# Kernel tuning notes

Hardware: AMD Instinct MI355X
Metric: run time of the kernel (lower is better)

## Reference

```python
import jax, jax.numpy as jnp
import numpy as np

N_NODES = 100000
N_EDGES = 1600000
HIDDEN = 64
N_MID = 3  # num_layers=5 -> 1 first + 3 middle + 1 last


def setup_inputs() -> dict:
    key = jax.random.key(0)
    ks = jax.random.split(key, 12)
    x = jax.random.normal(ks[0], (N_NODES, 1), dtype=jnp.float32)
    edge_index = jax.random.randint(ks[1], (2, N_EDGES), 0, N_NODES, dtype=jnp.int32)
    edge_weight = jax.random.uniform(ks[2], (N_EDGES,), dtype=jnp.float32)
    s0 = 1.0  # fan_in=1
    sh = 1.0 / np.sqrt(HIDDEN)
    Wrel0 = jax.random.normal(ks[3], (HIDDEN, 1), dtype=jnp.float32) * s0
    brel0 = jax.random.normal(ks[4], (HIDDEN,), dtype=jnp.float32) * s0
    Wroot0 = jax.random.normal(ks[5], (HIDDEN, 1), dtype=jnp.float32) * s0
    Wrel_mid = jax.random.normal(ks[6], (N_MID, HIDDEN, HIDDEN), dtype=jnp.float32) * sh
    brel_mid = jax.random.normal(ks[7], (N_MID, HIDDEN), dtype=jnp.float32) * sh
    Wroot_mid = jax.random.normal(ks[8], (N_MID, HIDDEN, HIDDEN), dtype=jnp.float32) * sh
    WrelL = jax.random.normal(ks[9], (1, HIDDEN), dtype=jnp.float32) * sh
    brelL = jax.random.normal(ks[10], (1,), dtype=jnp.float32) * sh
    WrootL = jax.random.normal(ks[11], (1, HIDDEN), dtype=jnp.float32) * sh
    return {"x": x, "edge_index": edge_index, "edge_weight": edge_weight,
            "Wrel0": Wrel0, "brel0": brel0, "Wroot0": Wroot0,
            "Wrel_mid": Wrel_mid, "brel_mid": brel_mid, "Wroot_mid": Wroot_mid,
            "WrelL": WrelL, "brelL": brelL, "WrootL": WrootL}


def reference(x, edge_index, edge_weight, Wrel0, brel0, Wroot0,
              Wrel_mid, brel_mid, Wroot_mid, WrelL, brelL, WrootL):
    src = edge_index[0]
    dst = edge_index[1]
    n = x.shape[0]

    def conv(h, Wrel, brel, Wroot):
        # PyG GraphConv(aggr='add'): lin_rel(sum_j w_ij * h_j) + lin_root(h_i)
        msg = h[src] * edge_weight[:, None]          # [E, C]
        agg = jax.ops.segment_sum(msg, dst, num_segments=n)  # [N, C]
        return agg @ Wrel.T + brel + h @ Wroot.T

    # dropout omitted (deterministic reference); relu after all but last layer
    h = jax.nn.relu(conv(x, Wrel0, brel0, Wroot0))
    for i in range(Wrel_mid.shape[0]):
        h = jax.nn.relu(conv(h, Wrel_mid[i], brel_mid[i], Wroot_mid[i]))
    return conv(h, WrelL, brelL, WrootL)  # [N, 1]
```

## Files before the change

### kernel.cpp

```cpp
#include <hip/hip_runtime.h>
#include <stdint.h>


#define NN 100000
#define NE 1600000
#define HID 64
#define NBKT 391
#define CAP 8192
#define TILE 4096
#define EPT 16
#define NTILE ((NE + TILE - 1) / TILE)

typedef __attribute__((ext_vector_type(8))) short bf16x8;
typedef __attribute__((ext_vector_type(4))) float f32x4;
typedef __attribute__((ext_vector_type(2))) unsigned int u32x2;
typedef __attribute__((ext_vector_type(4))) unsigned int u32x4;

__device__ __forceinline__ uint32_t rne_bf16(float v) {
    uint32_t u = __float_as_uint(v);
    return (u + 0x7fffu + ((u >> 16) & 1u)) >> 16;
}


__global__ __launch_bounds__(256) void k_bpart(const int* __restrict__ src,
                                               const int* __restrict__ dst,
                                               const float* __restrict__ w,
                                               int* __restrict__ bcur,
                                               int2* __restrict__ bpairs) {
    __shared__ int  hcnt[NBKT];
    __shared__ int  hoff[NBKT];
    __shared__ int  hadj[NBKT];
    __shared__ int  sc0[512];
    __shared__ int  sc1[512];
    __shared__ int2 sT[TILE];
    __shared__ int  sAdj[TILE];
    int tile0 = blockIdx.x * TILE;
    int t = threadIdx.x;
    for (int i = t; i < NBKT; i += 256) hcnt[i] = 0;
    __syncthreads();

    int   pk[EPT];
    int   bk[EPT];
    float wv[EPT];
    #pragma unroll
    for (int k = 0; k < EPT; k++) {
        int e = tile0 + t + k * 256;
        if (e < NE) {
            int d = dst[e];
            int b = d >> 8;
            pk[k] = (src[e] << 8) | (d & 255);
            wv[k] = w[e];
            bk[k] = b;
            atomicAdd(&hcnt[b], 1);
        } else {
            bk[k] = -1;
        }
    }
    __syncthreads();

    sc0[t]       = (t < NBKT) ? hcnt[t] : 0;
    sc0[t + 256] = (t + 256 < NBKT) ? hcnt[t + 256] : 0;
    __syncthreads();
    int* cur = sc0;
    int* oth = sc1;
    for (int off = 1; off < 512; off <<= 1) {
        int v0 = cur[t]       + ((t       >= off) ? cur[t - off]       : 0);
        int v1 = cur[t + 256] + ((t + 256 >= off) ? cur[t + 256 - off] : 0);
        oth[t] = v0;
        oth[t + 256] = v1;
        __syncthreads();
        int* tmp = cur; cur = oth; oth = tmp;
    }
    for (int i = t; i < NBKT; i += 256) {
        int c = hcnt[i];
        int excl = cur[i] - c;
        hoff[i] = excl;
        int gbase = c ? atomicAdd(&bcur[i], c) : 0;
        hadj[i] = gbase - excl;
        hcnt[i] = 0;
    }
    __syncthreads();

    #pragma unroll
    for (int k = 0; k < EPT; k++) {
        if (bk[k] >= 0) {
            int b = bk[k];
            int pos = hoff[b] + atomicAdd(&hcnt[b], 1);
            sT[pos] = make_int2(pk[k], __float_as_int(wv[k]));
            sAdj[pos] = hadj[b];
        }
    }
    __syncthreads();

    int n = NE - tile0; if (n > TILE) n = TILE;
    for (int j = t; j < n; j += 256)
        bpairs[sAdj[j] + j] = sT[j];
}

__global__ __launch_bounds__(256) void k_bcsr(const int* __restrict__ bcur,
                                              const int2* __restrict__ bpairs,
                                              int* __restrict__ offs,
                                              int* __restrict__ ends,
                                              uint32_t* __restrict__ pairs) {
    __shared__ int2 sE[CAP];
    __shared__ int cnt[256];
    __shared__ int scn[256];
    __shared__ int cur[256];
    int k = blockIdx.x, t = threadIdx.x;
    int base = k * CAP;
    int scnt = bcur[k] - base;
    cnt[t] = 0;
    __syncthreads();
    for (int j = t; j < scnt; j += 256) {
        int2 q = bpairs[base + j];
        sE[j] = q;
        atomicAdd(&cnt[q.x & 255], 1);
    }
    __syncthreads();
    int v = cnt[t], acc = v;
    scn[t] = v;
    __syncthreads();
    for (int off = 1; off < 256; off <<= 1) {
        int u = (t >= off) ? scn[t - off] : 0;
        __syncthreads();
        acc += u;
        scn[t] = acc;
        __syncthreads();
    }
    int excl = acc - v;
    cur[t] = excl;
    int d = (k << 8) + t;
    if (d < NN) {
        offs[d] = base + excl;
        ends[d] = base + excl + v;
    }
    __syncthreads();
    for (int j = t; j < scnt; j += 256) {
        int2 q = sE[j];
        int pos = base + atomicAdd(&cur[q.x & 255], 1);
        uint32_t wb = rne_bf16(__int_as_float(q.y)) & 0x7fffu;
        pairs[pos] = (wb << 17) | (uint32_t)(q.x >> 8);
    }
}


__global__ __launch_bounds__(256) void k_wsplit(const float* __restrict__ Wrel_mid,
                                                const float* __restrict__ Wroot_mid,
                                                uint16_t* __restrict__ WgH,
                                                uint16_t* __restrict__ WgL,
                                                uint16_t* __restrict__ WrH,
                                                uint16_t* __restrict__ WrL,
                                                int* __restrict__ bcur) {
    int i = blockIdx.x * blockDim.x + threadIdx.x;
    if (i < NBKT) bcur[i] = i * CAP;
    if (i >= 3 * 4096) return;
    float a = Wrel_mid[i];
    uint32_t ah = rne_bf16(a);
    float al = a - __uint_as_float(ah << 16);
    WgH[i] = (uint16_t)ah;
    WgL[i] = (uint16_t)rne_bf16(al);
    float b = Wroot_mid[i];
    uint32_t bh = rne_bf16(b);
    float bl = b - __uint_as_float(bh << 16);
    WrH[i] = (uint16_t)bh;
    WrL[i] = (uint16_t)rne_bf16(bl);
}


__device__ __forceinline__ void mfma_epilogue(
        int lane, int w, const uint32_t* sH,
        const uint16_t* __restrict__ WgH, const uint16_t* __restrict__ WgL,
        const uint16_t* __restrict__ WrH, const uint16_t* __restrict__ WrL,
        const float* __restrict__ brel,
        uint16_t* sG, uint16_t* sR) {
    int row = lane & 15;
    int quad = lane >> 4;
    int kb = quad * 8;
    bf16x8 ah0 = *(const bf16x8*)&sH[row * 36 + quad * 4];
    bf16x8 ah1 = *(const bf16x8*)&sH[row * 36 + 16 + quad * 4];
    int oc = w * 16 + row;
    {
        bf16x8 bh0 = *(const bf16x8*)&WgH[oc * 64 + kb];
        bf16x8 bh1 = *(const bf16x8*)&WgH[oc * 64 + 32 + kb];
        bf16x8 bl0 = *(const bf16x8*)&WgL[oc * 64 + kb];
        bf16x8 bl1 = *(const bf16x8*)&WgL[oc * 64 + 32 + kb];
        f32x4 acc = {0.f, 0.f, 0.f, 0.f};
        acc = __builtin_amdgcn_mfma_f32_16x16x32_bf16(ah0, bh0, acc, 0, 0, 0);
        acc = __builtin_amdgcn_mfma_f32_16x16x32_bf16(ah1, bh1, acc, 0, 0, 0);
        acc = __builtin_amdgcn_mfma_f32_16x16x32_bf16(ah0, bl0, acc, 0, 0, 0);
        acc = __builtin_amdgcn_mfma_f32_16x16x32_bf16(ah1, bl1, acc, 0, 0, 0);
        #pragma unroll
        for (int r = 0; r < 4; r++)
            sG[(quad * 4 + r) * 68 + oc] = (uint16_t)rne_bf16(acc[r]);
    }
    {
        bf16x8 bh0 = *(const bf16x8*)&WrH[oc * 64 + kb];
        bf16x8 bh1 = *(const bf16x8*)&WrH[oc * 64 + 32 + kb];
        bf16x8 bl0 = *(const bf16x8*)&WrL[oc * 64 + kb];
        bf16x8 bl1 = *(const bf16x8*)&WrL[oc * 64 + 32 + kb];
        float bias = brel[oc];
        f32x4 acc = {bias, bias, bias, bias};
        acc = __builtin_amdgcn_mfma_f32_16x16x32_bf16(ah0, bh0, acc, 0, 0, 0);
        acc = __builtin_amdgcn_mfma_f32_16x16x32_bf16(ah1, bh1, acc, 0, 0, 0);
        acc = __builtin_amdgcn_mfma_f32_16x16x32_bf16(ah0, bl0, acc, 0, 0, 0);
        acc = __builtin_amdgcn_mfma_f32_16x16x32_bf16(ah1, bl1, acc, 0, 0, 0);
        #pragma unroll
        for (int r = 0; r < 4; r++)
            sR[(quad * 4 + r) * 68 + oc] = (uint16_t)rne_bf16(acc[r]);
    }
}

__device__ __forceinline__ void epilogue_writeout(
        int tid, int blk16, const uint16_t* sG, const uint16_t* sR,
        uint16_t* __restrict__ Gout, uint16_t* __restrict__ Rout) {
    const uint32_t* sGd = (const uint32_t*)sG;
    const uint32_t* sRd = (const uint32_t*)sR;
    uint32_t* Gd = (uint32_t*)Gout;
    uint32_t* Rd = (uint32_t*)Rout;
    #pragma unroll
    for (int it = 0; it < 2; it++) {
        int idx = it * 256 + tid;
        int nd = idx >> 5, col = idx & 31;
        Gd[(blk16 + nd) * 32 + col] = sGd[nd * 34 + col];
        Rd[(blk16 + nd) * 32 + col] = sRd[nd * 34 + col];
    }
}


__global__ __launch_bounds__(256) void k_l0pre(
        const int* __restrict__ offs, const int* __restrict__ ends,
        const uint32_t* __restrict__ pairs, const float* __restrict__ x,
        const float* __restrict__ Wrel0, const float* __restrict__ brel0,
        const float* __restrict__ Wroot0,
        const uint16_t* __restrict__ WgH, const uint16_t* __restrict__ WgL,
        const uint16_t* __restrict__ WrH, const uint16_t* __restrict__ WrL,
        const float* __restrict__ brel,
        uint16_t* __restrict__ Gout, uint16_t* __restrict__ Rout) {
    __shared__ uint32_t sH[16 * 36];
    __shared__ uint16_t sG[16 * 68];
    __shared__ uint16_t sR[16 * 68];
    int c = threadIdx.x & 63;
    int w = threadIdx.x >> 6;
    int blk16 = blockIdx.x * 16;
    float agg[4];
    #pragma unroll
    for (int t = 0; t < 4; t++) {
        int node = blk16 + w * 4 + t;
        int b = offs[node], e = ends[node];
        float pp = 0.f;
        for (int j = b + c; j < e; j += 64) {
            uint32_t r = pairs[j];
            pp += __uint_as_float((r >> 17) << 16) * x[r & 0x1ffffu];
        }
        for (int o = 32; o > 0; o >>= 1) pp += __shfl_down(pp, o, 64);
        agg[t] = __shfl(pp, 0, 64);
    }
    float wr = Wrel0[c], br = brel0[c], wo = Wroot0[c];
    #pragma unroll
    for (int t = 0; t < 4; t++) {
        int node = blk16 + w * 4 + t;
        float v = agg[t] * wr + br + x[node] * wo;
        v = v > 0.f ? v : 0.f;
        uint32_t hb = rne_bf16(v);
        uint32_t pn = (uint32_t)__shfl_xor((int)hb, 1, 64);
        if (!(c & 1)) sH[(w * 4 + t) * 36 + (c >> 1)] = hb | (pn << 16);
    }
    __syncthreads();
    mfma_epilogue(c, w, sH, WgH, WgL, WrH, WrL, brel, sG, sR);
    __syncthreads();
    epilogue_writeout((int)threadIdx.x, blk16, sG, sR, Gout, Rout);
}

#define TRR(dst, off) \
    asm volatile("ds_read_b64_tr_b16 %0, %1 offset:" #off \
                 : "=v"(dst) : "v"(trb))

template <bool LAST>
__global__ __launch_bounds__(256, 6) void k_aggfused(
        const int* __restrict__ offs, const int* __restrict__ ends,
        const uint32_t* __restrict__ pairs,
        const uint16_t* __restrict__ Gb, const uint16_t* __restrict__ Rb,
        const uint16_t* __restrict__ WgH, const uint16_t* __restrict__ WgL,
        const uint16_t* __restrict__ WrH, const uint16_t* __restrict__ WrL,
        const float* __restrict__ brel,
        uint16_t* __restrict__ Gout, uint16_t* __restrict__ Rout,
        const float* __restrict__ WrelL, const float* __restrict__ WrootL,
        float* __restrict__ sarr, float* __restrict__ rarr) {
    __shared__ uint32_t sH[16 * 36];
    __shared__ __align__(128) char smem[16384];
    int c = threadIdx.x & 63;
    int w = threadIdx.x >> 6;
    int blk16 = blockIdx.x * 16;
    int n0 = blk16 + w * 4;
    int ov = 0;
    if (c < 4) ov = offs[n0 + c];
    else if (c == 4) ov = ends[n0 + 3];
    int bnd[5];
    bnd[0] = __builtin_amdgcn_readlane(ov, 0);
    bnd[1] = __builtin_amdgcn_readlane(ov, 1);
    bnd[2] = __builtin_amdgcn_readlane(ov, 2);
    bnd[3] = __builtin_amdgcn_readlane(ov, 3);
    bnd[4] = __builtin_amdgcn_readlane(ov, 4);

    int arow  = c & 15;
    int kq    = (c >> 4) * 8;
    int eprm  = ((c >> 5) << 2) | ((c >> 1) & 3);
    int lbyte = ((c >> 3) & 3) * 32 + (c & 1) * 16;
    char* stg = smem + w * 4096;
    uint32_t stgOff = (uint32_t)(uintptr_t)
        (__attribute__((address_space(3))) char*)stg;
    uint32_t trb = stgOff + ((uint32_t)(c >> 4) << 10)
                          + ((uint32_t)(c & 15) << 3);

    int blo = bnd[0], bhi = bnd[1];
    if (arow == 1) { blo = bnd[1]; bhi = bnd[2]; }
    if (arow == 2) { blo = bnd[2]; bhi = bnd[3]; }
    if (arow == 3) { blo = bnd[3]; bhi = bnd[4]; }
    if (arow >= 4) { blo = 0;      bhi = 0;      }
    uint32_t wid = (uint32_t)(bhi - blo);

    {
        f32x4 z = {0.f, 0.f, 0.f, 0.f};
        #pragma unroll
        for (int i = 0; i < 4; i++)
            *(f32x4*)(stg + i * 1024 + c * 16) = z;
        asm volatile("s_waitcnt lgkmcnt(0)" ::: "memory");
    }

    f32x4 acc16[4];
    {
        int ur[4];
        #pragma unroll
        for (int t = 0; t < 4; t++) ur[t] = (int)(uint32_t)Rb[(n0 + t) * 64 + c];
        #pragma unroll
        for (int nb = 0; nb < 4; nb++) {
            int idx = (nb * 16 + (c & 15)) * 4;
            f32x4 ci;
            #pragma unroll
            for (int t = 0; t < 4; t++) {
                uint32_t rv = (uint32_t)__builtin_amdgcn_ds_bpermute(idx, ur[t]);
                ci[t] = __uint_as_float(rv << 16);
            }
            acc16[nb] = ci;
        }
    }

    const char* gbase = (const char*)Gb;
    uint32_t p = 0;
    if (bnd[0] + c < bnd[4]) p = pairs[bnd[0] + c];

    for (int cb = bnd[0]; cb < bnd[4]; cb += 64) {
        uint32_t pnext = 0;
        if (cb + 64 + c < bnd[4]) pnext = pairs[cb + 64 + c];
        #pragma unroll
        for (int s = 0; s < 2; s++) {
            int sb = cb + s * 32;
            if (sb < bnd[4]) {
                int sn = bnd[4] - sb; if (sn > 32) sn = 32;
                int ni = (sn + 7) >> 3;
                int es4 = (s * 32 + eprm) * 4;
                #pragma unroll
                for (int i = 0; i < 4; i++) {
                    if (i < ni) {
                        uint32_t r = (uint32_t)__builtin_amdgcn_ds_bpermute(
                            es4 + i * 32, (int)p);
                        uint32_t voff = ((r & 0x1ffffu) << 7) + (uint32_t)lbyte;
                        __builtin_amdgcn_global_load_lds(
                            (const __attribute__((address_space(1))) void*)(gbase + voff),
                            (__attribute__((address_space(3))) void*)(stg + i * 1024),
                            16, 0, 0);
                    }
                }
                asm volatile("s_waitcnt vmcnt(0)" ::: "memory");
                u32x2 tb0, tb1, tb2, tb3, tb4, tb5, tb6, tb7;
                TRR(tb0, 0);   TRR(tb1, 512);
                TRR(tb2, 128); TRR(tb3, 640);
                TRR(tb4, 256); TRR(tb5, 768);
                TRR(tb6, 384); TRR(tb7, 896);
                int kidx = s * 128 + kq * 4;
                int db = sb + kq - blo;
                uint32_t m[8];
                #pragma unroll
                for (int q = 0; q < 8; q++) {
                    uint32_t rq = (uint32_t)__builtin_amdgcn_ds_bpermute(
                        kidx + q * 4, (int)p);
                    uint32_t bf = rq >> 17;
                    m[q] = ((uint32_t)(db + q) < wid) ? bf : 0u;
                }
                u32x4 aa = { m[0] | (m[1] << 16), m[2] | (m[3] << 16),
                             m[4] | (m[5] << 16), m[6] | (m[7] << 16) };
                bf16x8 af = __builtin_bit_cast(bf16x8, aa);
                asm volatile("s_waitcnt lgkmcnt(0)" ::: "memory");
                __builtin_amdgcn_sched_barrier(0);
                {
                    u32x4 bb0 = { tb0.x, tb0.y, tb1.x, tb1.y };
                    acc16[0] = __builtin_amdgcn_mfma_f32_16x16x32_bf16(
                        af, __builtin_bit_cast(bf16x8, bb0), acc16[0], 0, 0, 0);
                    u32x4 bb1 = { tb2.x, tb2.y, tb3.x, tb3.y };
                    acc16[1] = __builtin_amdgcn_mfma_f32_16x16x32_bf16(
                        af, __builtin_bit_cast(bf16x8, bb1), acc16[1], 0, 0, 0);
                    u32x4 bb2 = { tb4.x, tb4.y, tb5.x, tb5.y };
                    acc16[2] = __builtin_amdgcn_mfma_f32_16x16x32_bf16(
                        af, __builtin_bit_cast(bf16x8, bb2), acc16[2], 0, 0, 0);
                    u32x4 bb3 = { tb6.x, tb6.y, tb7.x, tb7.y };
                    acc16[3] = __builtin_amdgcn_mfma_f32_16x16x32_bf16(
                        af, __builtin_bit_cast(bf16x8, bb3), acc16[3], 0, 0, 0);
                }
            }
        }
        p = pnext;
    }

    if (!LAST) {
        #pragma unroll
        for (int t = 0; t < 4; t++) {
            #pragma unroll
            for (int nb = 0; nb < 4; nb++) {
                float v = acc16[nb][t];
                v = v > 0.f ? v : 0.f;
                uint32_t hb = rne_bf16(v);
                uint32_t pn2 = (uint32_t)__shfl_xor((int)hb, 1, 64);
                if (!(c & 1) && c < 16)
                    sH[(w * 4 + t) * 36 + nb * 8 + (c >> 1)] = hb | (pn2 << 16);
            }
        }
        __syncthreads();
        uint16_t* sG = (uint16_t*)smem;
        uint16_t* sR = (uint16_t*)(smem + 2176);
        mfma_epilogue(c, w, sH, WgH, WgL, WrH, WrL, brel, sG, sR);
        __syncthreads();
        epilogue_writeout((int)threadIdx.x, blk16, sG, sR, Gout, Rout);
    } else {
        float wl[4], wo[4];
        #pragma unroll
        for (int nb = 0; nb < 4; nb++) {
            wl[nb] = WrelL[nb * 16 + (c & 15)];
            wo[nb] = WrootL[nb * 16 + (c & 15)];
        }
        #pragma unroll
        for (int t = 0; t < 4; t++) {
            float pa = 0.f, pr = 0.f;
            #pragma unroll
            for (int nb = 0; nb < 4; nb++) {
                float v = acc16[nb][t];
                v = v > 0.f ? v : 0.f;
                pa += v * wl[nb];
                pr += v * wo[nb];
            }
            #pragma unroll
            for (int o = 8; o > 0; o >>= 1) {
                pa += __shfl_down(pa, o, 64);
                pr += __shfl_down(pr, o, 64);
            }
            if (c == 0) { sarr[n0 + t] = pa; rarr[n0 + t] = pr; }
        }
    }
}

__global__ void k_last(const int* __restrict__ offs, const int* __restrict__ ends,
                       const uint32_t* __restrict__ pairs,
                       const float* __restrict__ sarr, const float* __restrict__ rarr,
                       const float* __restrict__ brelL, float* __restrict__ out) {
    int i = blockIdx.x * blockDim.x + threadIdx.x;
    if (i >= NN) return;
    float a0 = rarr[i] + brelL[0], a1 = 0.f;
    int b = offs[i], e = ends[i];
    int j = b;
    for (; j + 2 <= e; j += 2) {
        uint32_t r0 = pairs[j], r1 = pairs[j + 1];
        a0 += __uint_as_float((r0 >> 17) << 16) * sarr[r0 & 0x1ffffu];
        a1 += __uint_as_float((r1 >> 17) << 16) * sarr[r1 & 0x1ffffu];
    }
    for (; j < e; j++) {
        uint32_t r = pairs[j];
        a0 += __uint_as_float((r >> 17) << 16) * sarr[r & 0x1ffffu];
    }
    out[i] = a0 + a1;
}

extern "C" void kernel_launch(void* const* d_in, const int* in_sizes, int n_in,
                              void* d_out, int out_size, void* d_ws, size_t ws_size,
                              hipStream_t stream) {
    const float* x        = (const float*)d_in[0];
    const int*   ei       = (const int*)d_in[1];
    const float* ew       = (const float*)d_in[2];
    const float* Wrel0    = (const float*)d_in[3];
    const float* brel0    = (const float*)d_in[4];
    const float* Wroot0   = (const float*)d_in[5];
    const float* Wrel_mid = (const float*)d_in[6];
    const float* brel_mid = (const float*)d_in[7];
    const float* Wroot_mid= (const float*)d_in[8];
    const float* WrelL    = (const float*)d_in[9];
    const float* brelL    = (const float*)d_in[10];
    const float* WrootL   = (const float*)d_in[11];
    float* out = (float*)d_out;

    const int* src  = ei;
    const int* dstp = ei + NE;

    char* w = (char*)d_ws;
    size_t o = 0;
    auto alloc = [&](size_t b) -> void* {
        void* r = (void*)(w + o);
        o += (b + 255) & ~(size_t)255;
        return r;
    };
    int*      offs  = (int*)alloc((size_t)NN * 4);
    int*      ends  = (int*)alloc((size_t)NN * 4);
    int*      bcur  = (int*)alloc((size_t)NBKT * 4);
    uint16_t* WgH   = (uint16_t*)alloc((size_t)3 * 4096 * 2);
    uint16_t* WgL   = (uint16_t*)alloc((size_t)3 * 4096 * 2);
    uint16_t* WrH   = (uint16_t*)alloc((size_t)3 * 4096 * 2);
    uint16_t* WrL   = (uint16_t*)alloc((size_t)3 * 4096 * 2);
    float*    sarr  = (float*)alloc((size_t)NN * 4);
    float*    rarr  = (float*)alloc((size_t)NN * 4);
    uint32_t* pairs = (uint32_t*)alloc((size_t)NBKT * CAP * 4);
    uint16_t* GbA   = (uint16_t*)alloc((size_t)NN * HID * 2);
    uint16_t* RbA   = (uint16_t*)alloc((size_t)NN * HID * 2);
    uint16_t* GbB   = (uint16_t*)alloc((size_t)NN * HID * 2);
    uint16_t* RbB   = (uint16_t*)alloc((size_t)NN * HID * 2);
    (void)RbB;
    int2*  bpairs = (int2*)GbB;

    k_wsplit<<<(3 * 4096 + 255) / 256, 256, 0, stream>>>(
        Wrel_mid, Wroot_mid, WgH, WgL, WrH, WrL, bcur);

    k_bpart<<<NTILE, 256, 0, stream>>>(src, dstp, ew, bcur, bpairs);
    k_bcsr<<<NBKT, 256, 0, stream>>>(bcur, bpairs, offs, ends, pairs);

    k_l0pre<<<NN / 16, 256, 0, stream>>>(
        offs, ends, pairs, x, Wrel0, brel0, Wroot0,
        WgH, WgL, WrH, WrL, brel_mid, GbA, RbA);

    k_aggfused<false><<<NN / 16, 256, 0, stream>>>(
        offs, ends, pairs, GbA, RbA,
        WgH + 4096, WgL + 4096, WrH + 4096, WrL + 4096, brel_mid + HID,
        GbB, RbB, WrelL, WrootL, sarr, rarr);
    k_aggfused<false><<<NN / 16, 256, 0, stream>>>(
        offs, ends, pairs, GbB, RbB,
        WgH + 2 * 4096, WgL + 2 * 4096, WrH + 2 * 4096, WrL + 2 * 4096,
        brel_mid + 2 * HID, GbA, RbA, WrelL, WrootL, sarr, rarr);
    k_aggfused<true><<<NN / 16, 256, 0, stream>>>(
        offs, ends, pairs, GbA, RbA,
        WgH, WgL, WrH, WrL, brel_mid,
        GbB, RbB, WrelL, WrootL, sarr, rarr);

    k_last<<<(NN + 255) / 256, 256, 0, stream>>>(offs, ends, pairs, sarr, rarr, brelL, out);
}
```

Before: 319.9 us.

## Double-buffer edge gathers in aggregation loop and warp-per-node final layer

The fused aggregation loop now issues both 32-edge halves of each 64-edge chunk into two separate LDS staging buffers before waiting. It then consumes the first half after a partial vmcnt wait while the second half's loads are still in flight. Per-half guards and the staging-buffer zero-fill are gone; out-of-range lanes gather row 0 and are masked through zero weights, and the pairs prefetch index is clamped. Doubling LDS per block lowers the occupancy hint from 6 to 4, and k_last is rewritten so each wavefront reduces one node's edges cooperatively instead of one thread per node.

Measured after the change: 324.4 us. Within noise of the previous version (+1.4%).

```diff
diff --git a/kernel.cpp b/kernel.cpp
--- a/kernel.cpp
+++ b/kernel.cpp
@@ -7,6 +7,7 @@
 #define HID 64
 #define NBKT 391
 #define CAP 8192
+#define PMAX (NBKT * CAP)
 #define TILE 4096
 #define EPT 16
 #define NTILE ((NE + TILE - 1) / TILE)
@@ -271,12 +272,15 @@
     epilogue_writeout((int)threadIdx.x, blk16, sG, sR, Gout, Rout);
 }
 
-#define TRR(dst, off) \
+#define TRRA(dst, off) \
     asm volatile("ds_read_b64_tr_b16 %0, %1 offset:" #off \
-                 : "=v"(dst) : "v"(trb))
+                 : "=v"(dst) : "v"(trbA))
+#define TRRB(dst, off) \
+    asm volatile("ds_read_b64_tr_b16 %0, %1 offset:" #off \
+                 : "=v"(dst) : "v"(trbB))
 
 template <bool LAST>
-__global__ __launch_bounds__(256, 6) void k_aggfused(
+__global__ __launch_bounds__(256, 4) void k_aggfused(
         const int* __restrict__ offs, const int* __restrict__ ends,
         const uint32_t* __restrict__ pairs,
         const uint16_t* __restrict__ Gb, const uint16_t* __restrict__ Rb,
@@ -287,7 +291,7 @@
         const float* __restrict__ WrelL, const float* __restrict__ WrootL,
         float* __restrict__ sarr, float* __restrict__ rarr) {
     __shared__ uint32_t sH[16 * 36];
-    __shared__ __align__(128) char smem[16384];
+    __shared__ __align__(128) char smem[32768];
     int c = threadIdx.x & 63;
     int w = threadIdx.x >> 6;
     int blk16 = blockIdx.x * 16;
@@ -306,11 +310,12 @@
     int kq    = (c >> 4) * 8;
     int eprm  = ((c >> 5) << 2) | ((c >> 1) & 3);
     int lbyte = ((c >> 3) & 3) * 32 + (c & 1) * 16;
-    char* stg = smem + w * 4096;
+    char* stg = smem + w * 8192;
     uint32_t stgOff = (uint32_t)(uintptr_t)
         (__attribute__((address_space(3))) char*)stg;
-    uint32_t trb = stgOff + ((uint32_t)(c >> 4) << 10)
+    uint32_t trbA = stgOff + ((uint32_t)(c >> 4) << 10)
                           + ((uint32_t)(c & 15) << 3);
+    uint32_t trbB = trbA + 4096;
 
     int blo = bnd[0], bhi = bnd[1];
     if (arow == 1) { blo = bnd[1]; bhi = bnd[2]; }
@@ -318,14 +323,6 @@
     if (arow == 3) { blo = bnd[3]; bhi = bnd[4]; }
     if (arow >= 4) { blo = 0;      bhi = 0;      }
     uint32_t wid = (uint32_t)(bhi - blo);
-
-    {
-        f32x4 z = {0.f, 0.f, 0.f, 0.f};
-        #pragma unroll
-        for (int i = 0; i < 4; i++)
-            *(f32x4*)(stg + i * 1024 + c * 16) = z;
-        asm volatile("s_waitcnt lgkmcnt(0)" ::: "memory");
-    }
 
     f32x4 acc16[4];
     {
@@ -346,69 +343,99 @@
     }
 
     const char* gbase = (const char*)Gb;
-    uint32_t p = 0;
-    if (bnd[0] + c < bnd[4]) p = pairs[bnd[0] + c];
+    int j0 = bnd[0] + c; if (j0 > PMAX - 1) j0 = PMAX - 1;
+    uint32_t praw = pairs[j0];
+    uint32_t p = (bnd[0] + c < bnd[4]) ? praw : 0;
 
     for (int cb = bnd[0]; cb < bnd[4]; cb += 64) {
-        uint32_t pnext = 0;
-        if (cb + 64 + c < bnd[4]) pnext = pairs[cb + 64 + c];
-        #pragma unroll
-        for (int s = 0; s < 2; s++) {
-            int sb = cb + s * 32;
-            if (sb < bnd[4]) {
-                int sn = bnd[4] - sb; if (sn > 32) sn = 32;
-                int ni = (sn + 7) >> 3;
-                int es4 = (s * 32 + eprm) * 4;
-                #pragma unroll
-                for (int i = 0; i < 4; i++) {
-                    if (i < ni) {
-                        uint32_t r = (uint32_t)__builtin_amdgcn_ds_bpermute(
-                            es4 + i * 32, (int)p);
-                        uint32_t voff = ((r & 0x1ffffu) << 7) + (uint32_t)lbyte;
-                        __builtin_amdgcn_global_load_lds(
-                            (const __attribute__((address_space(1))) void*)(gbase + voff),
-                            (__attribute__((address_space(3))) void*)(stg + i * 1024),
-                            16, 0, 0);
-                    }
-                }
-                asm volatile("s_waitcnt vmcnt(0)" ::: "memory");
-                u32x2 tb0, tb1, tb2, tb3, tb4, tb5, tb6, tb7;
-                TRR(tb0, 0);   TRR(tb1, 512);
-                TRR(tb2, 128); TRR(tb3, 640);
-                TRR(tb4, 256); TRR(tb5, 768);
-                TRR(tb6, 384); TRR(tb7, 896);
-                int kidx = s * 128 + kq * 4;
-                int db = sb + kq - blo;
-                uint32_t m[8];
-                #pragma unroll
-                for (int q = 0; q < 8; q++) {
-                    uint32_t rq = (uint32_t)__builtin_amdgcn_ds_bpermute(
-                        kidx + q * 4, (int)p);
-                    uint32_t bf = rq >> 17;
-                    m[q] = ((uint32_t)(db + q) < wid) ? bf : 0u;
-                }
-                u32x4 aa = { m[0] | (m[1] << 16), m[2] | (m[3] << 16),
-                             m[4] | (m[5] << 16), m[6] | (m[7] << 16) };
-                bf16x8 af = __builtin_bit_cast(bf16x8, aa);
-                asm volatile("s_waitcnt lgkmcnt(0)" ::: "memory");
-                __builtin_amdgcn_sched_barrier(0);
-                {
-                    u32x4 bb0 = { tb0.x, tb0.y, tb1.x, tb1.y };
-                    acc16[0] = __builtin_amdgcn_mfma_f32_16x16x32_bf16(
-                        af, __builtin_bit_cast(bf16x8, bb0), acc16[0], 0, 0, 0);
-                    u32x4 bb1 = { tb2.x, tb2.y, tb3.x, tb3.y };
-                    acc16[1] = __builtin_amdgcn_mfma_f32_16x16x32_bf16(
-                        af, __builtin_bit_cast(bf16x8, bb1), acc16[1], 0, 0, 0);
-                    u32x4 bb2 = { tb4.x, tb4.y, tb5.x, tb5.y };
-                    acc16[2] = __builtin_amdgcn_mfma_f32_16x16x32_bf16(
-                        af, __builtin_bit_cast(bf16x8, bb2), acc16[2], 0, 0, 0);
-                    u32x4 bb3 = { tb6.x, tb6.y, tb7.x, tb7.y };
-                    acc16[3] = __builtin_amdgcn_mfma_f32_16x16x32_bf16(
-                        af, __builtin_bit_cast(bf16x8, bb3), acc16[3], 0, 0, 0);
-                }
-            }
-        }
-        p = pnext;
+        int jn = cb + 64 + c; if (jn > PMAX - 1) jn = PMAX - 1;
+        uint32_t pr2 = pairs[jn];
+        #pragma unroll
+        for (int i = 0; i < 4; i++) {
+            uint32_t r = (uint32_t)__builtin_amdgcn_ds_bpermute(
+                (eprm + i * 8) * 4, (int)p);
+            uint32_t voff = ((r & 0x1ffffu) << 7) + (uint32_t)lbyte;
+            __builtin_amdgcn_global_load_lds(
+                (const __attribute__((address_space(1))) void*)(gbase + voff),
+                (__attribute__((address_space(3))) void*)(stg + i * 1024),
+                16, 0, 0);
+        }
+        #pragma unroll
+        for (int i = 0; i < 4; i++) {
+            uint32_t r = (uint32_t)__builtin_amdgcn_ds_bpermute(
+                (32 + eprm + i * 8) * 4, (int)p);
+            uint32_t voff = ((r & 0x1ffffu) << 7) + (uint32_t)lbyte;
+            __builtin_amdgcn_global_load_lds(
+                (const __attribute__((address_space(1))) void*)(gbase + voff),
+                (__attribute__((address_space(3))) void*)(stg + 4096 + i * 1024),
+                16, 0, 0);
+        }
+        uint32_t mA[8], mB[8];
+        int dbA = cb + kq - blo;
+        int dbB = cb + 32 + kq - blo;
+        #pragma unroll
+        for (int q = 0; q < 8; q++) {
+            uint32_t rq = (uint32_t)__builtin_amdgcn_ds_bpermute(
+                (kq + q) * 4, (int)p);
+            mA[q] = ((uint32_t)(dbA + q) < wid) ? (rq >> 17) : 0u;
+        }
+        #pragma unroll
+        for (int q = 0; q < 8; q++) {
+            uint32_t rq = (uint32_t)__builtin_amdgcn_ds_bpermute(
+                (32 + kq + q) * 4, (int)p);
+            mB[q] = ((uint32_t)(dbB + q) < wid) ? (rq >> 17) : 0u;
+        }
+        u32x4 aav = { mA[0] | (mA[1] << 16), mA[2] | (mA[3] << 16),
+                      mA[4] | (mA[5] << 16), mA[6] | (mA[7] << 16) };
+        u32x4 abv = { mB[0] | (mB[1] << 16), mB[2] | (mB[3] << 16),
+                      mB[4] | (mB[5] << 16), mB[6] | (mB[7] << 16) };
+        bf16x8 afA = __builtin_bit_cast(bf16x8, aav);
+        bf16x8 afB = __builtin_bit_cast(bf16x8, abv);
+        asm volatile("s_waitcnt vmcnt(4)" ::: "memory");
+        {
+            u32x2 tb0, tb1, tb2, tb3, tb4, tb5, tb6, tb7;
+            TRRA(tb0, 0);   TRRA(tb1, 512);
+            TRRA(tb2, 128); TRRA(tb3, 640);
+            TRRA(tb4, 256); TRRA(tb5, 768);
+            TRRA(tb6, 384); TRRA(tb7, 896);
+            asm volatile("s_waitcnt lgkmcnt(0)" ::: "memory");
+            __builtin_amdgcn_sched_barrier(0);
+            u32x4 bb0 = { tb0.x, tb0.y, tb1.x, tb1.y };
+            acc16[0] = __builtin_amdgcn_mfma_f32_16x16x32_bf16(
+                afA, __builtin_bit_cast(bf16x8, bb0), acc16[0], 0, 0, 0);
+            u32x4 bb1 = { tb2.x, tb2.y, tb3.x, tb3.y };
+            acc16[1] = __builtin_amdgcn_mfma_f32_16x16x32_bf16(
+                afA, __builtin_bit_cast(bf16x8, bb1), acc16[1], 0, 0, 0);
+            u32x4 bb2 = { tb4.x, tb4.y, tb5.x, tb5.y };
+            acc16[2] = __builtin_amdgcn_mfma_f32_16x16x32_bf16(
+                afA, __builtin_bit_cast(bf16x8, bb2), acc16[2], 0, 0, 0);
+            u32x4 bb3 = { tb6.x, tb6.y, tb7.x, tb7.y };
+            acc16[3] = __builtin_amdgcn_mfma_f32_16x16x32_bf16(
+                afA, __builtin_bit_cast(bf16x8, bb3), acc16[3], 0, 0, 0);
+        }
+        asm volatile("s_waitcnt vmcnt(0)" ::: "memory");
+        {
+            u32x2 tb0, tb1, tb2, tb3, tb4, tb5, tb6, tb7;
+            TRRB(tb0, 0);   TRRB(tb1, 512);
+            TRRB(tb2, 128); TRRB(tb3, 640);
+            TRRB(tb4, 256); TRRB(tb5, 768);
+            TRRB(tb6, 384); TRRB(tb7, 896);
+            asm volatile("s_waitcnt lgkmcnt(0)" ::: "memory");
+            __builtin_amdgcn_sched_barrier(0);
+            u32x4 bb0 = { tb0.x, tb0.y, tb1.x, tb1.y };
+            acc16[0] = __builtin_amdgcn_mfma_f32_16x16x32_bf16(
+                afB, __builtin_bit_cast(bf16x8, bb0), acc16[0], 0, 0, 0);
+            u32x4 bb1 = { tb2.x, tb2.y, tb3.x, tb3.y };
+            acc16[1] = __builtin_amdgcn_mfma_f32_16x16x32_bf16(
+                afB, __builtin_bit_cast(bf16x8, bb1), acc16[1], 0, 0, 0);
+            u32x4 bb2 = { tb4.x, tb4.y, tb5.x, tb5.y };
+            acc16[2] = __builtin_amdgcn_mfma_f32_16x16x32_bf16(
+                afB, __builtin_bit_cast(bf16x8, bb2), acc16[2], 0, 0, 0);
+            u32x4 bb3 = { tb6.x, tb6.y, tb7.x, tb7.y };
+            acc16[3] = __builtin_amdgcn_mfma_f32_16x16x32_bf16(
+                afB, __builtin_bit_cast(bf16x8, bb3), acc16[3], 0, 0, 0);
+        }
+        p = (cb + 64 + c < bnd[4]) ? pr2 : 0;
     }
 
     if (!LAST) {
@@ -457,25 +484,28 @@
     }
 }
 
-__global__ void k_last(const int* __restrict__ offs, const int* __restrict__ ends,
-                       const uint32_t* __restrict__ pairs,
-                       const float* __restrict__ sarr, const float* __restrict__ rarr,
-                       const float* __restrict__ brelL, float* __restrict__ out) {
-    int i = blockIdx.x * blockDim.x + threadIdx.x;
-    if (i >= NN) return;
-    float a0 = rarr[i] + brelL[0], a1 = 0.f;
-    int b = offs[i], e = ends[i];
-    int j = b;
-    for (; j + 2 <= e; j += 2) {
-        uint32_t r0 = pairs[j], r1 = pairs[j + 1];
-        a0 += __uint_as_float((r0 >> 17) << 16) * sarr[r0 & 0x1ffffu];
-        a1 += __uint_as_float((r1 >> 17) << 16) * sarr[r1 & 0x1ffffu];
-    }
-    for (; j < e; j++) {
-        uint32_t r = pairs[j];
-        a0 += __uint_as_float((r >> 17) << 16) * sarr[r & 0x1ffffu];
-    }
-    out[i] = a0 + a1;
+__global__ __launch_bounds__(256) void k_last(
+        const int* __restrict__ offs, const int* __restrict__ ends,
+        const uint32_t* __restrict__ pairs,
+        const float* __restrict__ sarr, const float* __restrict__ rarr,
+        const float* __restrict__ brelL, float* __restrict__ out) {
+    int c = threadIdx.x & 63;
+    int w = threadIdx.x >> 6;
+    int blk16 = blockIdx.x * 16;
+    float b0 = brelL[0];
+    #pragma unroll
+    for (int t = 0; t < 4; t++) {
+        int node = blk16 + w * 4 + t;
+        int b = offs[node], e = ends[node];
+        float pp = 0.f;
+        for (int j = b + c; j < e; j += 64) {
+            uint32_t r = pairs[j];
+            pp += __uint_as_float((r >> 17) << 16) * sarr[r & 0x1ffffu];
+        }
+        #pragma unroll
+        for (int o = 32; o > 0; o >>= 1) pp += __shfl_down(pp, o, 64);
+        if (c == 0) out[node] = pp + rarr[node] + b0;
+    }
 }
 
 extern "C" void kernel_launch(void* const* d_in, const int* in_sizes, int n_in,
@@ -545,5 +575,5 @@
         WgH, WgL, WrH, WrL, brel_mid,
         GbB, RbB, WrelL, WrootL, sarr, rarr);
 
-    k_last<<<(NN + 255) / 256, 256, 0, stream>>>(offs, ends, pairs, sarr, rarr, brelL, out);
-}
+    k_last<<<NN / 16, 256, 0, stream>>>(offs, ends, pairs, sarr, rarr, brelL, out);
+}
```
